# Optimization experiments

Measured on AMD Instinct MI355X. Metric: run time of the kernel, lower is better.

## Reference

```python
import jax, jax.numpy as jnp
import numpy as np

B, C, H, W = 4, 64, 256, 256
WS = 8          # window size
HEADS = 4       # dim // dim_head, dim_head = 16
DH = 16         # dim_head used for scale
HID = 64        # gated conv FFN hidden (mult=1)


def conv2d(x, w, b=None, stride=1, pad=1, groups=1):
    out = jax.lax.conv_general_dilated(
        x, w, (stride, stride), [(pad, pad), (pad, pad)],
        feature_group_count=groups,
        dimension_numbers=('NCHW', 'OIHW', 'NCHW'))
    if b is not None:
        out = out + b[None, :, None, None]
    return out


def gelu(x):
    return jax.nn.gelu(x, approximate=False)  # torch F.gelu / nn.GELU default (erf)


def ln2d(x, w, b, eps=1e-6):  # LayerNorm2d: normalize over channel dim
    mu = jnp.mean(x, axis=1, keepdims=True)
    var = jnp.mean((x - mu) ** 2, axis=1, keepdims=True)
    return w[None, :, None, None] * ((x - mu) / jnp.sqrt(var + eps)) + b[None, :, None, None]


def ln_last(x, w, b, eps=1e-5):  # nn.LayerNorm over last dim
    mu = jnp.mean(x, axis=-1, keepdims=True)
    var = jnp.mean((x - mu) ** 2, axis=-1, keepdims=True)
    return w * ((x - mu) / jnp.sqrt(var + eps)) + b


def to_windows(x, w):  # b d (x w1) (y w2) -> b x y w1 w2 d
    b, c, h, ww = x.shape
    x = x.reshape(b, c, h // w, w, ww // w, w)
    return jnp.transpose(x, (0, 2, 4, 3, 5, 1))


def from_windows(x):  # b x y w1 w2 d -> b d (x w1) (y w2)
    b, nx, ny, w1, w2, c = x.shape
    return jnp.transpose(x, (0, 5, 1, 3, 2, 4)).reshape(b, c, nx * w1, ny * w2)


def setup_inputs() -> dict:
    key = jax.random.key(0)
    ks = iter(jax.random.split(key, 64))

    def rn(*shape):
        return jax.random.normal(next(ks), shape, dtype=jnp.float32) * 0.05

    d = dict(
        x=jax.random.normal(next(ks), (B, C, H, W), dtype=jnp.float32),
        norm_w=jnp.ones((C,), jnp.float32), norm_b=jnp.zeros((C,), jnp.float32),
        conv1_w=rn(C, C, 1, 1), conv1_b=jnp.zeros((C,), jnp.float32),
        conv2_w=rn(C, 2 * C, 1, 1), conv2_b=jnp.zeros((C,), jnp.float32),
        mb_w1=rn(C, C, 1, 1), mb_b1=jnp.zeros((C,), jnp.float32),
        mb_dw_w=rn(C, 1, 3, 3), mb_dw_b=jnp.zeros((C,), jnp.float32),
        se_w1=rn(16, C), se_w2=rn(C, 16),
        mb_w2=rn(C, C, 1, 1), mb_b2=jnp.zeros((C,), jnp.float32),
        ln_att_w=jnp.ones((C,), jnp.float32), ln_att_b=jnp.zeros((C,), jnp.float32),
        q1_w=rn(C // 2, C), q1_b=jnp.zeros((C // 2,), jnp.float32),
        qkv_w=rn(3 * C // 2, C // 2),
        to_out_w=rn(C // 2, C // 2),
        sr_w=rn(C, C, 3, 3), sr_b=jnp.zeros((C,), jnp.float32),
        ln_sr_w=jnp.ones((C,), jnp.float32), ln_sr_b=jnp.zeros((C,), jnp.float32),
        kv1_w=rn(C, C), kv1_b=jnp.zeros((C,), jnp.float32),
        q2_w=rn(C // 2, C), q2_b=jnp.zeros((C // 2,), jnp.float32),
        cd_w=rn(C // 2, C // 2, 3, 3), cd_b=jnp.zeros((C // 2,), jnp.float32),
        cu_w=rn(C // 2, C // 2, 3, 3), cu_b=jnp.zeros((C // 2,), jnp.float32),
        cln1_w=jnp.ones((C,), jnp.float32), cln1_b=jnp.zeros((C,), jnp.float32),
        ff1_in_w=rn(2 * HID, C, 1, 1), ff1_dw_w=rn(2 * HID, 1, 3, 3), ff1_out_w=rn(C, HID, 1, 1),
        cln2_w=jnp.ones((C,), jnp.float32), cln2_b=jnp.zeros((C,), jnp.float32),
        ca_temp=jnp.ones((HEADS, 1, 1), jnp.float32),
        ca_qkv_w=rn(3 * C, C, 1, 1), ca_dw_w=rn(3 * C, 1, 3, 3), ca_out_w=rn(C, C, 1, 1),
        cln3_w=jnp.ones((C,), jnp.float32), cln3_b=jnp.zeros((C,), jnp.float32),
        ff2_in_w=rn(2 * HID, C, 1, 1), ff2_dw_w=rn(2 * HID, 1, 3, 3), ff2_out_w=rn(C, HID, 1, 1),
    )
    return d


def reference(x, norm_w, norm_b, conv1_w, conv1_b, conv2_w, conv2_b,
              mb_w1, mb_b1, mb_dw_w, mb_dw_b, se_w1, se_w2, mb_w2, mb_b2,
              ln_att_w, ln_att_b, q1_w, q1_b, qkv_w, to_out_w,
              sr_w, sr_b, ln_sr_w, ln_sr_b, kv1_w, kv1_b, q2_w, q2_b,
              cd_w, cd_b, cu_w, cu_b,
              cln1_w, cln1_b, ff1_in_w, ff1_dw_w, ff1_out_w,
              cln2_w, cln2_b, ca_temp, ca_qkv_w, ca_dw_w, ca_out_w,
              cln3_w, cln3_b, ff2_in_w, ff2_dw_w, ff2_out_w):
    scale = DH ** -0.5
    # input norm + 1x1 conv
    y = conv2d(ln2d(x, norm_w, norm_b), conv1_w, conv1_b, pad=0)
    # ---- MBConv (expansion 1, SE, residual) ----
    r = y
    t = gelu(conv2d(y, mb_w1, mb_b1, pad=0))
    t = gelu(conv2d(t, mb_dw_w, mb_dw_b, pad=1, groups=C))
    s = jnp.mean(t, axis=(2, 3))                      # (B,C) squeeze
    s = jax.nn.sigmoid(jax.nn.silu(s @ se_w1.T) @ se_w2.T)
    y = conv2d(t * s[:, :, None, None], mb_w2, mb_b2, pad=0) + r
    # ---- windowed hybrid attention, PreNormResidual ----
    xw = to_windows(y, WS)                            # (B,nx,ny,8,8,C)
    xn = ln_last(xw, ln_att_w, ln_att_b)
    xf = from_windows(xn)                             # (B,C,H,W)
    b, c, h, w = xf.shape
    nx, ny = h // WS, w // WS
    # window self-attention branch on dim/2
    xq = jnp.einsum('bchw,oc->bohw', xf, q1_w) + q1_b[None, :, None, None]
    tw = to_windows(xq, WS).reshape(b * nx * ny, WS * WS, c // 2)
    qkv = tw @ qkv_w.T
    q, k, v = jnp.split(qkv, 3, axis=-1)

    def heads_split(t):
        return jnp.transpose(t.reshape(t.shape[0], WS * WS, HEADS, -1), (0, 2, 1, 3))

    q, k, v = heads_split(q) * scale, heads_split(k), heads_split(v)
    attn = jax.nn.softmax(jnp.einsum('bhid,bhjd->bhij', q, k), axis=-1)
    o = jnp.einsum('bhij,bhjd->bhid', attn, v)
    o = jnp.transpose(o, (0, 2, 1, 3)).reshape(b * nx * ny, WS, WS, c // 2)
    o = (o @ to_out_w.T).reshape(b, nx, ny, WS, WS, c // 2)
    # low-resolution cross-attention branch on dim/2
    iq = jnp.einsum('bchw,oc->bohw', xf, q2_w) + q2_b[None, :, None, None]
    iq = conv2d(iq, cd_w, cd_b, stride=8, pad=1)      # (B,C/2,H/8,W/8)
    qq = jnp.transpose(iq.reshape(b, h * w // 64, HEADS // 2, c // HEADS), (0, 2, 1, 3))
    x1 = conv2d(xf, sr_w, sr_b, stride=16, pad=1)     # (B,C,h16,w16)
    x1 = jnp.transpose(x1.reshape(b, c, -1), (0, 2, 1))
    x1 = gelu(ln_last(x1, ln_sr_w, ln_sr_b))
    kv = (x1 @ kv1_w.T + kv1_b).reshape(b, -1, 2, HEADS // 2, c // HEADS)
    kv = jnp.transpose(kv, (2, 0, 3, 1, 4))
    k1, v1 = kv[0], kv[1]                             # (B,2,N,16)
    a1 = jax.nn.softmax(jnp.einsum('bhid,bhjd->bhij', qq, k1) * scale, axis=-1)
    o1 = jnp.einsum('bhij,bhjd->bhid', a1, v1)        # (B,2,HW/64,16)
    o1 = jnp.transpose(o1, (0, 1, 3, 2)).reshape(b, c // 2, h // 8, w // 8)
    o1 = jnp.repeat(jnp.repeat(o1, 8, axis=2), 8, axis=3)   # nearest upsample x8
    o1 = to_windows(conv2d(o1, cu_w, cu_b, pad=1), WS)
    xw = jnp.concatenate([o, o1], axis=-1) + xw       # residual
    y = from_windows(xw)

    def gcff(z, in_w, dw_w, out_w):
        t = conv2d(conv2d(z, in_w, pad=0), dw_w, pad=1, groups=2 * HID)
        a, g = jnp.split(t, 2, axis=1)
        return conv2d(gelu(a) * g, out_w, pad=0)

    y = y + gcff(ln2d(y, cln1_w, cln1_b), ff1_in_w, ff1_dw_w, ff1_out_w)
    # ---- windowed channel (transposed) attention ----
    z = ln2d(y, cln2_w, cln2_b)
    qkv2 = conv2d(conv2d(z, ca_qkv_w, pad=0), ca_dw_w, pad=1, groups=3 * C)
    qc, kc, vc = jnp.split(qkv2, 3, axis=1)
    hp, wp = h // WS, w // WS

    def rw(t):  # b (head d) (h ph) (w pw) -> b (h w) head d (ph pw)
        t = t.reshape(b, HEADS, C // HEADS, hp, WS, wp, WS)
        return jnp.transpose(t, (0, 3, 5, 1, 2, 4, 6)).reshape(b, hp * wp, HEADS, C // HEADS, WS * WS)

    qc, kc, vc = rw(qc), rw(kc), rw(vc)
    qc = qc / jnp.clip(jnp.linalg.norm(qc, axis=-1, keepdims=True), 1e-12)
    kc = kc / jnp.clip(jnp.linalg.norm(kc, axis=-1, keepdims=True), 1e-12)
    aat = jax.nn.softmax(jnp.einsum('bnhde,bnhfe->bnhdf', qc, kc) * ca_temp, axis=-1)
    oc = jnp.einsum('bnhdf,bnhfe->bnhde', aat, vc)    # (B,Nw,head,16,64)
    oc = oc.reshape(b, hp, wp, HEADS, C // HEADS, WS, WS)
    oc = jnp.transpose(oc, (0, 3, 4, 1, 5, 2, 6)).reshape(b, C, h, w)
    y = y + conv2d(oc, ca_out_w, pad=0)
    y = y + gcff(ln2d(y, cln3_w, cln3_b), ff2_in_w, ff2_dw_w, ff2_out_w)
    # fuse branch with block input
    return conv2d(jnp.concatenate([x, y], axis=1), conv2_w, conv2_b, pad=0)
```

## Files before the change

kernel.cpp:

```cpp
#include <hip/hip_runtime.h>
#include <hip/hip_bf16.h>
#include <math.h>

typedef __hip_bfloat16 bf16;

static constexpr int B_ = 4;
static constexpr int C_ = 64;
static constexpr int H_ = 256;
static constexpr int W_ = 256;
static constexpr int P_ = H_ * W_;
static constexpr int NP_ = B_ * P_;

static constexpr int HSTR = 61;

__device__ __forceinline__ float cvt(float x) { return x; }
__device__ __forceinline__ float cvt(bf16 x) { return __bfloat162float(x); }
__device__ __forceinline__ float geluf(float x) { return 0.5f * x * (1.0f + erff(x * 0.70710678118654752f)); }
__device__ __forceinline__ float sigm(float x) { return 1.0f / (1.0f + __expf(-x)); }

__device__ __forceinline__ float ldin(const void* p, int i, bool bf) {
    return bf ? __bfloat162float(((const bf16*)p)[i]) : ((const float*)p)[i];
}

__device__ __forceinline__ void bf2x(unsigned u, float& a, float& b) {
    a = __uint_as_float(u << 16);
    b = __uint_as_float(u & 0xffff0000u);
}
__device__ __forceinline__ float bflo(unsigned u) { return __uint_as_float(u << 16); }
__device__ __forceinline__ float bfhi(unsigned u) { return __uint_as_float(u & 0xffff0000u); }
__device__ __forceinline__ unsigned bfpack(float a, float b) {
    union { unsigned u; bf16 h[2]; } pk;
    pk.h[0] = __float2bfloat16(a);
    pk.h[1] = __float2bfloat16(b);
    return pk.u;
}

__device__ __forceinline__ int win_swz(int bid) { return (bid & 7) * 512 + (bid >> 3); }

__global__ __launch_bounds__(256) void k_detect(const unsigned int* __restrict__ x, int* __restrict__ flag) {
    __shared__ int red[256];
    int cnt = 0;
    for (int i = threadIdx.x; i < 4096; i += 256) {
        unsigned int u = x[i];
        unsigned int e = (u >> 7) & 0xFFu;
        cnt += (e >= 100u && e <= 140u) ? 1 : 0;
    }
    red[threadIdx.x] = cnt;
    __syncthreads();
    for (int s = 128; s > 0; s >>= 1) {
        if (threadIdx.x < s) red[threadIdx.x] += red[threadIdx.x + s];
        __syncthreads();
    }
    if (threadIdx.x == 0) flag[0] = (red[0] > 2048) ? 1 : 0;
}

__global__ __launch_bounds__(256) void k_head(const void* __restrict__ x,
                                              const void* __restrict__ lnw, const void* __restrict__ lnb,
                                              const void* __restrict__ w1, const void* __restrict__ b1,
                                              const void* __restrict__ w2, const void* __restrict__ b2,
                                              float* __restrict__ Y, bf16* __restrict__ T1,
                                              const int* __restrict__ dtf) {
    const bool bf = dtf[0] != 0;
    __shared__ bf16 s1[4096], s2[4096];
    __shared__ float sb1[64], sb2[64], slw[64], slb[64];
    for (int i = threadIdx.x; i < 4096; i += 256) {
        s1[i] = __float2bfloat16(ldin(w1, i, bf));
        s2[i] = __float2bfloat16(ldin(w2, i, bf));
    }
    if (threadIdx.x < 64) {
        sb1[threadIdx.x] = ldin(b1, threadIdx.x, bf);
        sb2[threadIdx.x] = ldin(b2, threadIdx.x, bf);
        slw[threadIdx.x] = ldin(lnw, threadIdx.x, bf);
        slb[threadIdx.x] = ldin(lnb, threadIdx.x, bf);
    }
    __syncthreads();
    int g = blockIdx.x * 256 + threadIdx.x;
    int bb = g >> 16, p = g & (P_ - 1);
    int base = bb * 64 * P_ + p;
    float v[64];
    float mu = 0.f;
#pragma unroll
    for (int c = 0; c < 64; ++c) { v[c] = ldin(x, base + c * P_, bf); mu += v[c]; }
    mu *= (1.0f / 64.0f);
    float var = 0.f;
#pragma unroll
    for (int c = 0; c < 64; ++c) { float d = v[c] - mu; var += d * d; }
    float inv = rsqrtf(var * (1.0f / 64.0f) + 1e-6f);
#pragma unroll
    for (int c = 0; c < 64; ++c) v[c] = (v[c] - mu) * inv * slw[c] + slb[c];
    float y[64];
    const unsigned* u1 = (const unsigned*)s1;
    for (int o = 0; o < 64; ++o) {
        float a = sb1[o];
#pragma unroll
        for (int cc = 0; cc < 32; ++cc) {
            float wa, wb;
            bf2x(u1[o * 32 + cc], wa, wb);
            a = fmaf(wa, v[2 * cc], fmaf(wb, v[2 * cc + 1], a));
        }
        y[o] = a;
        Y[base + o * P_] = a;
    }
    const unsigned* u2 = (const unsigned*)s2;
    for (int o = 0; o < 64; ++o) {
        float a = sb2[o];
#pragma unroll
        for (int cc = 0; cc < 32; ++cc) {
            float wa, wb;
            bf2x(u2[o * 32 + cc], wa, wb);
            a = fmaf(wa, y[2 * cc], fmaf(wb, y[2 * cc + 1], a));
        }
        T1[base + o * P_] = __float2bfloat16(geluf(a));
    }
}

__global__ __launch_bounds__(256) void k_ln(const float* __restrict__ in,
                                            const void* __restrict__ w,
                                            const void* __restrict__ b,
                                            bf16* __restrict__ out, float eps,
                                            const int* __restrict__ dtf) {
    const bool bf = dtf[0] != 0;
    __shared__ float swt[C_], sbt[C_];
    if (threadIdx.x < C_) {
        swt[threadIdx.x] = ldin(w, threadIdx.x, bf);
        sbt[threadIdx.x] = ldin(b, threadIdx.x, bf);
    }
    __syncthreads();
    int g = blockIdx.x * 256 + threadIdx.x;
    int bb = g >> 16;
    int p = g & (P_ - 1);
    int base = bb * C_ * P_ + p;
    float v[C_];
    float mu = 0.f;
#pragma unroll
    for (int c = 0; c < C_; ++c) { v[c] = in[base + c * P_]; mu += v[c]; }
    mu *= (1.0f / C_);
    float var = 0.f;
#pragma unroll
    for (int c = 0; c < C_; ++c) { float d = v[c] - mu; var += d * d; }
    var *= (1.0f / C_);
    float inv = rsqrtf(var + eps);
#pragma unroll
    for (int c = 0; c < C_; ++c)
        out[base + c * P_] = __float2bfloat16((v[c] - mu) * inv * swt[c] + sbt[c]);
}

template <int COUT>
__global__ __launch_bounds__(256) void k_pwln(const float* __restrict__ Yin,
                                              const void* __restrict__ lnw, const void* __restrict__ lnb,
                                              const void* __restrict__ w,
                                              bf16* __restrict__ out,
                                              const int* __restrict__ dtf) {
    const bool bf = dtf[0] != 0;
    __shared__ bf16 swb[COUT * 64];
    __shared__ float slw[64], slb[64];
    for (int i = threadIdx.x; i < COUT * 64; i += 256) swb[i] = __float2bfloat16(ldin(w, i, bf));
    if (threadIdx.x < 64) {
        slw[threadIdx.x] = ldin(lnw, threadIdx.x, bf);
        slb[threadIdx.x] = ldin(lnb, threadIdx.x, bf);
    }
    __syncthreads();
    int g = blockIdx.x * 256 + threadIdx.x;
    int bb = g >> 16, p = g & (P_ - 1);
    int base = bb * 64 * P_ + p;
    float v[64];
    float mu = 0.f;
#pragma unroll
    for (int c = 0; c < 64; ++c) { v[c] = Yin[base + c * P_]; mu += v[c]; }
    mu *= (1.0f / 64.0f);
    float var = 0.f;
#pragma unroll
    for (int c = 0; c < 64; ++c) { float d = v[c] - mu; var += d * d; }
    float inv = rsqrtf(var * (1.0f / 64.0f) + 1e-6f);
#pragma unroll
    for (int c = 0; c < 64; ++c) v[c] = (v[c] - mu) * inv * slw[c] + slb[c];
    int obase = bb * COUT * P_ + p;
    const unsigned* uw = (const unsigned*)swb;
    for (int o = 0; o < COUT; ++o) {
        float a = 0.f;
#pragma unroll
        for (int cc = 0; cc < 32; ++cc) {
            float wa, wb;
            bf2x(uw[o * 32 + cc], wa, wb);
            a = fmaf(wa, v[2 * cc], fmaf(wb, v[2 * cc + 1], a));
        }
        out[obase + o * P_] = __float2bfloat16(a);
    }
}

__global__ __launch_bounds__(256) void k_dwmean(const bf16* __restrict__ h,
                                                const void* __restrict__ dww,
                                                const void* __restrict__ dwb,
                                                float* __restrict__ part,
                                                const int* __restrict__ dtf) {
    const bool bf = dtf[0] != 0;
    __shared__ __align__(8) bf16 hsb[10 * 256];
    __shared__ float red[256];
    int bid = blockIdx.x;
    int bc = bid >> 5, chunk = bid & 31;
    int c = bc & 63;
    int h0 = chunk * 8;
    int base = bc * P_;
    int tid = threadIdx.x;
    {
        const unsigned* gq = (const unsigned*)h;
        unsigned* hu = (unsigned*)hsb;
        for (int i = tid; i < 1280; i += 256) {
            int r = i >> 7, col2 = i & 127;
            int hh = h0 - 1 + r;
            unsigned v = 0u;
            if ((unsigned)hh < (unsigned)H_) v = gq[(base + hh * W_) / 2 + col2];
            hu[r * 128 + col2] = v;
        }
    }
    float w9[9];
#pragma unroll
    for (int k = 0; k < 9; ++k) w9[k] = ldin(dww, c * 9 + k, bf);
    float bv = ldin(dwb, c, bf);
    __syncthreads();
    float acc = 0.f;
#pragma unroll
    for (int k = 0; k < 8; ++k) {
        int j = tid + k * 256;
        int r = j >> 8, x = j & 255;
        float s = bv;
#pragma unroll
        for (int kh = 0; kh < 3; ++kh) {
            const bf16* row = &hsb[(r + kh) * 256];
            float vm1 = (x > 0) ? cvt(row[x - 1]) : 0.f;
            float v0 = cvt(row[x]);
            float vp1 = (x < 255) ? cvt(row[x + 1]) : 0.f;
            s = fmaf(w9[kh * 3 + 0], vm1, s);
            s = fmaf(w9[kh * 3 + 1], v0, s);
            s = fmaf(w9[kh * 3 + 2], vp1, s);
        }
        acc += geluf(s);
    }
    red[tid] = acc;
    __syncthreads();
    for (int s2 = 128; s2 > 0; s2 >>= 1) {
        if (tid < s2) red[tid] += red[tid + s2];
        __syncthreads();
    }
    if (tid == 0) part[bc * 32 + chunk] = red[0];
}

__global__ __launch_bounds__(256) void k_se(const float* __restrict__ part,
                                            const void* __restrict__ w1,
                                            const void* __restrict__ w2,
                                            float* __restrict__ sfin,
                                            const int* __restrict__ dtf) {
    const bool bf = dtf[0] != 0;
    __shared__ float ssum[256];
    __shared__ float hbuf[B_ * 16];
    int t = threadIdx.x;
    {
        float a = 0.f;
#pragma unroll
        for (int k = 0; k < 32; ++k) a += part[t * 32 + k];
        ssum[t] = a * (1.0f / P_);
    }
    __syncthreads();
    if (t < B_ * 16) {
        int bb = t >> 4, j = t & 15;
        float a = 0.f;
        for (int c = 0; c < 64; ++c) a = fmaf(ssum[bb * 64 + c], ldin(w1, j * 64 + c, bf), a);
        hbuf[t] = a * sigm(a);
    }
    __syncthreads();
    int bb = t >> 6, c = t & 63;
    float a = 0.f;
    for (int j = 0; j < 16; ++j) a = fmaf(hbuf[bb * 16 + j], ldin(w2, c * 16 + j, bf), a);
    sfin[t] = sigm(a);
}

__global__ __launch_bounds__(256) void k_mb2w(const bf16* __restrict__ h,
                                              const void* __restrict__ dww, const void* __restrict__ dwb,
                                              const void* __restrict__ w2, const void* __restrict__ b2,
                                              const float* __restrict__ sfin,
                                              float* __restrict__ Y,
                                              const int* __restrict__ dtf) {
    const bool bf = dtf[0] != 0;
    __shared__ __align__(16) bf16 hs[64 * 2 * HSTR];
    __shared__ __align__(16) bf16 ts[64 * 66];
    __shared__ __align__(16) bf16 sw2T[64 * 64];
    __shared__ float sdb[64], sb2[64], ssc[64];
    int wid = win_swz(blockIdx.x);
    int bb = wid >> 10;
    int h0 = ((wid >> 5) & 31) * 8, w0 = (wid & 31) * 8;
    int tid = threadIdx.x;
    int cch = tid >> 2, quarter = tid & 3;
    {
        const unsigned* gq = (const unsigned*)h;
        unsigned* hsu = (unsigned*)hs;
        int j = quarter * 15;
        int pr = j / 6, col = j - pr * 6;
        size_t chb = (size_t)(bb * 64 + cch) * P_;
        for (int k = 0; k < 15; ++k) {
            int hh = h0 + pr - 1;
            int wcx = w0 - 2 + 2 * col;
            unsigned v = 0u;
            if ((unsigned)hh < (unsigned)H_ && (unsigned)wcx < 255u)
                v = gq[(chb + hh * W_ + wcx) >> 1];
            hsu[cch * HSTR + j] = v;
            ++j; ++col;
            if (col == 6) { col = 0; ++pr; }
        }
    }
    float w9[9];
#pragma unroll
    for (int k = 0; k < 9; ++k) w9[k] = ldin(dww, cch * 9 + k, bf);
    for (int i = tid; i < 4096; i += 256) {
        int c = i >> 6, o = i & 63;
        sw2T[c * 64 + o] = __float2bfloat16(ldin(w2, o * 64 + c, bf));
    }
    if (tid < 64) {
        sdb[tid] = ldin(dwb, tid, bf);
        sb2[tid] = ldin(b2, tid, bf);
        ssc[tid] = sfin[bb * 64 + tid];
    }
    __syncthreads();
    {
        const unsigned* mua = (const unsigned*)hs + cch * HSTR;
        unsigned* tsu = (unsigned*)ts;
        float bv = sdb[cch];
        float sc = ssc[cch];
#pragma unroll
        for (int k = 0; k < 8; ++k) {
            int p = quarter * 8 + k;
            int t0 = 2 * p;
            int rt = t0 >> 3, ct = t0 & 7;
            float a0 = bv, a1 = bv;
#pragma unroll
            for (int kh = 0; kh < 3; ++kh) {
                int rb = (rt + kh) * 6 + (ct >> 1);
                unsigned u0 = mua[rb], u1 = mua[rb + 1], u2 = mua[rb + 2];
                float x1 = bfhi(u0);
                float x2 = bflo(u1), x3 = bfhi(u1);
                float x4 = bflo(u2);
                a0 = fmaf(w9[kh * 3 + 0], x1, fmaf(w9[kh * 3 + 1], x2, fmaf(w9[kh * 3 + 2], x3, a0)));
                a1 = fmaf(w9[kh * 3 + 0], x2, fmaf(w9[kh * 3 + 1], x3, fmaf(w9[kh * 3 + 2], x4, a1)));
            }
            tsu[cch * 33 + p] = bfpack(geluf(a0) * sc, geluf(a1) * sc);
        }
    }
    __syncthreads();
    int og = tid >> 4, pg = tid & 15;
    int o0 = og * 4, p0 = pg * 4;
    float acc[4][4] = {};
    const unsigned* wt = (const unsigned*)sw2T;
    const unsigned* tt = (const unsigned*)ts;
    for (int c = 0; c < 64; ++c) {
        float w0v, w1v, w2v, w3v, t0, t1, t2, t3;
        bf2x(wt[c * 32 + (o0 >> 1)], w0v, w1v);
        bf2x(wt[c * 32 + (o0 >> 1) + 1], w2v, w3v);
        bf2x(tt[c * 33 + (p0 >> 1)], t0, t1);
        bf2x(tt[c * 33 + (p0 >> 1) + 1], t2, t3);
        acc[0][0] = fmaf(w0v, t0, acc[0][0]); acc[0][1] = fmaf(w0v, t1, acc[0][1]);
        acc[0][2] = fmaf(w0v, t2, acc[0][2]); acc[0][3] = fmaf(w0v, t3, acc[0][3]);
        acc[1][0] = fmaf(w1v, t0, acc[1][0]); acc[1][1] = fmaf(w1v, t1, acc[1][1]);
        acc[1][2] = fmaf(w1v, t2, acc[1][2]); acc[1][3] = fmaf(w1v, t3, acc[1][3]);
        acc[2][0] = fmaf(w2v, t0, acc[2][0]); acc[2][1] = fmaf(w2v, t1, acc[2][1]);
        acc[2][2] = fmaf(w2v, t2, acc[2][2]); acc[2][3] = fmaf(w2v, t3, acc[2][3]);
        acc[3][0] = fmaf(w3v, t0, acc[3][0]); acc[3][1] = fmaf(w3v, t1, acc[3][1]);
        acc[3][2] = fmaf(w3v, t2, acc[3][2]); acc[3][3] = fmaf(w3v, t3, acc[3][3]);
    }
#pragma unroll
    for (int i = 0; i < 4; ++i)
#pragma unroll
        for (int j = 0; j < 4; ++j) {
            int t = p0 + j;
            int p = (h0 + (t >> 3)) * W_ + w0 + (t & 7);
            Y[(bb * 64 + o0 + i) * P_ + p] += acc[i][j] + sb2[o0 + i];
        }
}

__global__ __launch_bounds__(256) void k_wprep(const void* __restrict__ q1w, const void* __restrict__ q1b,
                                               const void* __restrict__ qkvw, const void* __restrict__ outw,
                                               bf16* __restrict__ WQT, float* __restrict__ BQ,
                                               bf16* __restrict__ OWT,
                                               const int* __restrict__ dtf) {
    const bool bf = dtf[0] != 0;
    __shared__ float sq1[32 * 64];
    __shared__ float sqk[96 * 32];
    __shared__ float sb1[32];
    int tid = threadIdx.x;
    for (int i = tid; i < 2048; i += 256) sq1[i] = ldin(q1w, i, bf);
    for (int i = tid; i < 3072; i += 256) sqk[i] = ldin(qkvw, i, bf);
    if (tid < 32) sb1[tid] = ldin(q1b, tid, bf);
    __syncthreads();
    for (int idx = tid; idx < 6144; idx += 256) {
        int o = idx % 96, c = idx / 96;
        float a = 0.f;
        for (int k = 0; k < 32; ++k) a = fmaf(sqk[o * 32 + k], sq1[k * 64 + c], a);
        if (o < 32) a *= 0.25f;
        WQT[c * 96 + o] = __float2bfloat16(a);
    }
    if (tid < 96) {
        float a = 0.f;
        for (int k = 0; k < 32; ++k) a = fmaf(sqk[tid * 32 + k], sb1[k], a);
        if (tid < 32) a *= 0.25f;
        BQ[tid] = a;
    }
    for (int idx = tid; idx < 1024; idx += 256) {
        int o = idx >> 5, c = idx & 31;
        OWT[c * 32 + o] = __float2bfloat16(ldin(outw, o * 32 + c, bf));
    }
}

__global__ __launch_bounds__(256, 4) void k_winattn(const bf16* __restrict__ xf,
                                                    const uint4* __restrict__ WQT,
                                                    const float* __restrict__ BQ,
                                                    const unsigned* __restrict__ OWT,
                                                    float* __restrict__ Y) {
    __shared__ __align__(16) char arena[35200];
    int wid = win_swz(blockIdx.x);
    int bb = wid >> 10;
    int h0 = ((wid >> 5) & 31) * 8, w0 = (wid & 31) * 8;
    int tid = threadIdx.x;
    {
        uint4* sW4 = (uint4*)arena;
        for (int i = tid; i < 768; i += 256) sW4[i] = WQT[i];
        if (tid < 96) ((float*)(arena + 12288))[tid] = BQ[tid];
#pragma unroll
        for (int k = 0; k < 2; ++k) {
            int idx = tid + k * 256;
            int c = idx >> 3, r = idx & 7;
            const uint4 v = *(const uint4*)(xf + (size_t)(bb * 64 + c) * P_ + (h0 + r) * W_ + w0);
            *(uint4*)(arena + 12672 + c * 144 + r * 16) = v;
        }
    }
    __syncthreads();
    {
        const unsigned* uW = (const unsigned*)arena;
        const float* sbq = (const float*)(arena + 12288);
        const unsigned* uX = (const unsigned*)(arena + 12672);
        unsigned* uQw = (unsigned*)(arena + 21888);
        int og = tid >> 4, pg = tid & 15;
        float acc[6][4];
#pragma unroll
        for (int i = 0; i < 6; ++i) {
            float b = sbq[og * 6 + i];
#pragma unroll
            for (int j = 0; j < 4; ++j) acc[i][j] = b;
        }
        for (int c = 0; c < 64; ++c) {
            unsigned wu0 = uW[c * 48 + 3 * og];
            unsigned wu1 = uW[c * 48 + 3 * og + 1];
            unsigned wu2 = uW[c * 48 + 3 * og + 2];
            unsigned xu0 = uX[c * 36 + 2 * pg];
            unsigned xu1 = uX[c * 36 + 2 * pg + 1];
            float wv[6], xv[4];
            bf2x(wu0, wv[0], wv[1]); bf2x(wu1, wv[2], wv[3]); bf2x(wu2, wv[4], wv[5]);
            bf2x(xu0, xv[0], xv[1]); bf2x(xu1, xv[2], xv[3]);
#pragma unroll
            for (int i = 0; i < 6; ++i)
#pragma unroll
                for (int j = 0; j < 4; ++j) acc[i][j] = fmaf(wv[i], xv[j], acc[i][j]);
        }
#pragma unroll
        for (int j = 0; j < 4; ++j) {
            int t = pg * 4 + j;
#pragma unroll
            for (int k = 0; k < 3; ++k) {
                union { unsigned u; bf16 h[2]; } pk;
                pk.h[0] = __float2bfloat16(acc[2 * k][j]);
                pk.h[1] = __float2bfloat16(acc[2 * k + 1][j]);
                uQw[t * 52 + 3 * og + k] = pk.u;
            }
        }
    }
    __syncthreads();
    {
        int hH = tid >> 6, lane = tid & 63;
        const unsigned* uQ = (const unsigned*)(arena + 21888);
        unsigned ow0 = OWT[tid * 2], ow1 = OWT[tid * 2 + 1];
        float qf[8];
        {
            const uint4 qv = *(const uint4*)&uQ[lane * 52 + hH * 4];
            bf2x(qv.x, qf[0], qf[1]); bf2x(qv.y, qf[2], qf[3]);
            bf2x(qv.z, qf[4], qf[5]); bf2x(qv.w, qf[6], qf[7]);
        }
        float p[64];
#pragma unroll
        for (int j = 0; j < 64; ++j) {
            const uint4 kv4 = *(const uint4*)&uQ[j * 52 + 16 + hH * 4];
            float kf[8];
            bf2x(kv4.x, kf[0], kf[1]); bf2x(kv4.y, kf[2], kf[3]);
            bf2x(kv4.z, kf[4], kf[5]); bf2x(kv4.w, kf[6], kf[7]);
            float s = 0.f;
#pragma unroll
            for (int d = 0; d < 8; ++d) s = fmaf(qf[d], kf[d], s);
            p[j] = s;
        }
        float m0 = fmaxf(p[0], p[4]), m1 = fmaxf(p[1], p[5]);
        float m2 = fmaxf(p[2], p[6]), m3 = fmaxf(p[3], p[7]);
#pragma unroll
        for (int j = 8; j < 64; j += 4) {
            m0 = fmaxf(m0, p[j]);     m1 = fmaxf(m1, p[j + 1]);
            m2 = fmaxf(m2, p[j + 2]); m3 = fmaxf(m3, p[j + 3]);
        }
        float mm = fmaxf(fmaxf(m0, m1), fmaxf(m2, m3));
        float s0 = 0.f, s1 = 0.f, s2 = 0.f, s3 = 0.f;
#pragma unroll
        for (int j = 0; j < 64; j += 4) {
            p[j] = __expf(p[j] - mm);         s0 += p[j];
            p[j + 1] = __expf(p[j + 1] - mm); s1 += p[j + 1];
            p[j + 2] = __expf(p[j + 2] - mm); s2 += p[j + 2];
            p[j + 3] = __expf(p[j + 3] - mm); s3 += p[j + 3];
        }
        float rs = 1.0f / ((s0 + s1) + (s2 + s3));
        float o[8] = {0.f, 0.f, 0.f, 0.f, 0.f, 0.f, 0.f, 0.f};
#pragma unroll
        for (int j = 0; j < 64; ++j) {
            const uint4 vv = *(const uint4*)&uQ[j * 52 + 32 + hH * 4];
            float vf[8];
            bf2x(vv.x, vf[0], vf[1]); bf2x(vv.y, vf[2], vf[3]);
            bf2x(vv.z, vf[4], vf[5]); bf2x(vv.w, vf[6], vf[7]);
#pragma unroll
            for (int d = 0; d < 8; ++d) o[d] = fmaf(p[j], vf[d], o[d]);
        }
        bf16* soa = (bf16*)(arena + 12672);
#pragma unroll
        for (int d = 0; d < 8; ++d)
            soa[(hH * 8 + d) * 68 + lane] = __float2bfloat16(o[d] * rs);
        unsigned* sow = (unsigned*)(arena + 17024);
        sow[tid * 2] = ow0; sow[tid * 2 + 1] = ow1;
    }
    __syncthreads();
    {
        const unsigned* uOW = (const unsigned*)(arena + 17024);
        const unsigned* uOA = (const unsigned*)(arena + 12672);
        int og = tid >> 4, pg = tid & 15;
        float a2[2][4] = {};
        for (int c = 0; c < 32; ++c) {
            unsigned wu = uOW[c * 16 + og];
            unsigned a0 = uOA[c * 34 + 2 * pg], a1 = uOA[c * 34 + 2 * pg + 1];
            float wf0, wf1, x0, x1, x2, x3;
            bf2x(wu, wf0, wf1); bf2x(a0, x0, x1); bf2x(a1, x2, x3);
            a2[0][0] = fmaf(wf0, x0, a2[0][0]); a2[0][1] = fmaf(wf0, x1, a2[0][1]);
            a2[0][2] = fmaf(wf0, x2, a2[0][2]); a2[0][3] = fmaf(wf0, x3, a2[0][3]);
            a2[1][0] = fmaf(wf1, x0, a2[1][0]); a2[1][1] = fmaf(wf1, x1, a2[1][1]);
            a2[1][2] = fmaf(wf1, x2, a2[1][2]); a2[1][3] = fmaf(wf1, x3, a2[1][3]);
        }
#pragma unroll
        for (int i = 0; i < 2; ++i)
#pragma unroll
            for (int j = 0; j < 4; ++j) {
                int t = pg * 4 + j;
                int p2 = (h0 + (t >> 3)) * W_ + w0 + (t & 7);
                Y[((size_t)bb * 64 + og * 2 + i) * P_ + p2] += a2[i][j];
            }
    }
}

template <int CIN, int COUT>
__global__ __launch_bounds__(256) void k_pw(const bf16* __restrict__ in,
                                            const void* __restrict__ w,
                                            const void* __restrict__ bias,
                                            bf16* __restrict__ out,
                                            const int* __restrict__ dtf) {
    const bool bf = dtf[0] != 0;
    __shared__ float sw[COUT * CIN];
    __shared__ float sb[COUT];
    for (int i = threadIdx.x; i < COUT * CIN; i += 256) sw[i] = ldin(w, i, bf);
    if (threadIdx.x < COUT) sb[threadIdx.x] = bias ? ldin(bias, threadIdx.x, bf) : 0.f;
    __syncthreads();
    int g = blockIdx.x * 256 + threadIdx.x;
    int bb = g >> 16;
    int p = g & (P_ - 1);
    int ibase = bb * CIN * P_ + p;
    float v[CIN];
#pragma unroll
    for (int c = 0; c < CIN; ++c) v[c] = cvt(in[ibase + c * P_]);
    int obase = bb * COUT * P_ + p;
    for (int o = 0; o < COUT; ++o) {
        float acc = sb[o];
        const float* wr = &sw[o * CIN];
#pragma unroll
        for (int c = 0; c < CIN; ++c) acc = fmaf(wr[c], v[c], acc);
        out[obase + o * P_] = __float2bfloat16(acc);
    }
}

template <int CIN, int COUT, int OS, int STRIDE>
__global__ __launch_bounds__(256) void k_sconv(const bf16* __restrict__ in,
                                               const void* __restrict__ w,
                                               const void* __restrict__ bias,
                                               float* __restrict__ out,
                                               const int* __restrict__ dtf) {
    const bool bf = dtf[0] != 0;
    int g = blockIdx.x * 256 + threadIdx.x;
    int ow = g % OS;
    int oh = (g / OS) % OS;
    int oc = (g / (OS * OS)) % COUT;
    int bb = g / (OS * OS * COUT);
    float acc = ldin(bias, oc, bf);
    for (int ic = 0; ic < CIN; ++ic) {
        int ibase = (bb * CIN + ic) * P_;
        int wbase = (oc * CIN + ic) * 9;
#pragma unroll
        for (int kh = 0; kh < 3; ++kh) {
            int ih = oh * STRIDE + kh - 1;
            if ((unsigned)ih >= (unsigned)H_) continue;
#pragma unroll
            for (int kw = 0; kw < 3; ++kw) {
                int iw = ow * STRIDE + kw - 1;
                if ((unsigned)iw >= (unsigned)W_) continue;
                acc = fmaf(ldin(w, wbase + kh * 3 + kw, bf), cvt(in[ibase + ih * W_ + iw]), acc);
            }
        }
    }
    out[g] = acc;
}

__global__ __launch_bounds__(64) void k_srkv(const float* __restrict__ x1,
                                             const void* __restrict__ lnw,
                                             const void* __restrict__ lnb,
                                             const void* __restrict__ kvw,
                                             const void* __restrict__ kvb,
                                             float* __restrict__ k1,
                                             float* __restrict__ v1,
                                             const int* __restrict__ dtf) {
    const bool bf = dtf[0] != 0;
    int tok = blockIdx.x;
    int bb = tok >> 8;
    int n = tok & 255;
    int c = threadIdx.x;
    __shared__ float sv[64];
    __shared__ float sg[64];
    float v = x1[(bb * 64 + c) * 256 + n];
    sv[c] = v;
    __syncthreads();
    float mu = 0.f;
    for (int i = 0; i < 64; ++i) mu += sv[i];
    mu *= (1.0f / 64.0f);
    float var = 0.f;
    for (int i = 0; i < 64; ++i) { float d = sv[i] - mu; var += d * d; }
    var *= (1.0f / 64.0f);
    float xn = (v - mu) * rsqrtf(var + 1e-5f) * ldin(lnw, c, bf) + ldin(lnb, c, bf);
    sg[c] = geluf(xn);
    __syncthreads();
    float acc = ldin(kvb, c, bf);
    for (int j = 0; j < 64; ++j) acc = fmaf(ldin(kvw, c * 64 + j, bf), sg[j], acc);
    int kk = c >> 5;
    int jh = (c >> 4) & 1;
    int d = c & 15;
    float* dst = kk ? v1 : k1;
    dst[((bb * 2 + jh) * 256 + n) * 16 + d] = acc;
}

__global__ __launch_bounds__(256) void k_xattn(const float* __restrict__ iqd,
                                               const float* __restrict__ k1,
                                               const float* __restrict__ v1,
                                               float* __restrict__ o1sp) {
    int bid = blockIdx.x;
    int iblk = bid & 3;
    int j = (bid >> 2) & 1;
    int bb = bid >> 3;
    __shared__ float sk[256 * 16];
    __shared__ float svv[256 * 16];
    int kbase = ((bb * 2 + j) * 256) * 16;
    for (int idx = threadIdx.x; idx < 4096; idx += 256) { sk[idx] = k1[kbase + idx]; svv[idx] = v1[kbase + idx]; }
    __syncthreads();
    int i = iblk * 256 + threadIdx.x;
    float q[16];
    int qbase = ((bb * 32 + (i >> 5)) * 32 + (i & 31)) * 32 + j * 16;
#pragma unroll
    for (int d = 0; d < 16; ++d) q[d] = iqd[qbase + d];
    float m = -1e30f, l = 0.f, o[16];
#pragma unroll
    for (int d = 0; d < 16; ++d) o[d] = 0.f;
    for (int n = 0; n < 256; ++n) {
        float s = 0.f;
#pragma unroll
        for (int d = 0; d < 16; ++d) s = fmaf(q[d], sk[n * 16 + d], s);
        s *= 0.25f;
        float mn = fmaxf(m, s);
        float corr = __expf(m - mn);
        float e = __expf(s - mn);
        l = l * corr + e;
#pragma unroll
        for (int d = 0; d < 16; ++d) o[d] = fmaf(o[d], corr, e * svv[n * 16 + d]);
        m = mn;
    }
    float r = 1.0f / l;
#pragma unroll
    for (int d = 0; d < 16; ++d)
        o1sp[((bb * 32 + j * 16 + d) * 32 + (i >> 5)) * 32 + (i & 31)] = o[d] * r;
}

__global__ __launch_bounds__(256) void k_cuconv(const float* __restrict__ o1sp,
                                                const void* __restrict__ w,
                                                const void* __restrict__ bias,
                                                float* __restrict__ Y,
                                                const int* __restrict__ dtf) {
    const bool bf = dtf[0] != 0;
    __shared__ float sw[32 * 32 * 9];
    for (int i = threadIdx.x; i < 9216; i += 256) sw[i] = ldin(w, i, bf);
    __syncthreads();
    int g = blockIdx.x * 256 + threadIdx.x;
    int bb = g >> 16;
    int p = g & 65535;
    int h = p >> 8, x = p & 255;
    float acc[32];
#pragma unroll
    for (int oc = 0; oc < 32; ++oc) acc[oc] = ldin(bias, oc, bf);
    for (int ic = 0; ic < 32; ++ic) {
        int ibase = (bb * 32 + ic) * 1024;
        float v[9];
#pragma unroll
        for (int kh = 0; kh < 3; ++kh)
#pragma unroll
            for (int kw = 0; kw < 3; ++kw) {
                int hh = h + kh - 1, ww = x + kw - 1;
                v[kh * 3 + kw] = ((unsigned)hh < (unsigned)H_ && (unsigned)ww < (unsigned)W_)
                                     ? o1sp[ibase + (hh >> 3) * 32 + (ww >> 3)] : 0.f;
            }
        for (int oc = 0; oc < 32; ++oc) {
            const float* wr = &sw[(oc * 32 + ic) * 9];
            float a = acc[oc];
#pragma unroll
            for (int k = 0; k < 9; ++k) a = fmaf(wr[k], v[k], a);
            acc[oc] = a;
        }
    }
#pragma unroll
    for (int oc = 0; oc < 32; ++oc) Y[(bb * 64 + 32 + oc) * P_ + p] += acc[oc];
}

__global__ __launch_bounds__(256) void k_gcff2(const bf16* __restrict__ mid_g,
                                               const void* __restrict__ dww,
                                               const void* __restrict__ outw,
                                               float* __restrict__ Y,
                                               const int* __restrict__ dtf) {
    const bool bf = dtf[0] != 0;
    __shared__ __align__(16) char arena[39680];
    bf16* mid = (bf16*)arena;
    bf16* ts = (bf16*)(arena + 31232);
    bf16* sowT = (bf16*)arena;
    int wid = win_swz(blockIdx.x);
    int bb = wid >> 10;
    int h0 = ((wid >> 5) & 31) * 8, w0 = (wid & 31) * 8;
    int tid = threadIdx.x;
    {
        const unsigned* gq = (const unsigned*)mid_g;
        unsigned* mu = (unsigned*)mid;
        int c = tid >> 1, half = tid & 1;
        int j = half * 30;
        int pr = half * 5, col = 0;
        size_t chb = (size_t)(bb * 128 + c) * P_;
        for (int k = 0; k < 30; ++k) {
            int hh = h0 + pr - 1;
            int wcx = w0 - 2 + 2 * col;
            unsigned v = 0u;
            if ((unsigned)hh < (unsigned)H_ && (unsigned)wcx < 255u)
                v = gq[(chb + hh * W_ + wcx) >> 1];
            mu[c * HSTR + j] = v;
            ++j; ++col;
            if (col == 6) { col = 0; ++pr; }
        }
    }
    int cch = tid >> 2, quarter = tid & 3;
    float wa9[9], wg9[9];
#pragma unroll
    for (int k = 0; k < 9; ++k) {
        wa9[k] = ldin(dww, cch * 9 + k, bf);
        wg9[k] = ldin(dww, (cch + 64) * 9 + k, bf);
    }
    __syncthreads();
    {
        const unsigned* mua = (const unsigned*)mid + cch * HSTR;
        const unsigned* mug = (const unsigned*)mid + (cch + 64) * HSTR;
        unsigned* tsu = (unsigned*)ts;
#pragma unroll
        for (int k = 0; k < 8; ++k) {
            int p = quarter * 8 + k;
            int t0 = 2 * p;
            int rt = t0 >> 3, ct = t0 & 7;
            float a0 = 0.f, a1 = 0.f, g0 = 0.f, g1 = 0.f;
#pragma unroll
            for (int kh = 0; kh < 3; ++kh) {
                int rb = (rt + kh) * 6 + (ct >> 1);
                unsigned ua0 = mua[rb], ua1 = mua[rb + 1], ua2 = mua[rb + 2];
                unsigned ug0 = mug[rb], ug1 = mug[rb + 1], ug2 = mug[rb + 2];
                float x1 = bfhi(ua0);
                float x2 = bflo(ua1), x3 = bfhi(ua1);
                float x4 = bflo(ua2);
                a0 = fmaf(wa9[kh * 3 + 0], x1, fmaf(wa9[kh * 3 + 1], x2, fmaf(wa9[kh * 3 + 2], x3, a0)));
                a1 = fmaf(wa9[kh * 3 + 0], x2, fmaf(wa9[kh * 3 + 1], x3, fmaf(wa9[kh * 3 + 2], x4, a1)));
                float y1 = bfhi(ug0);
                float y2 = bflo(ug1), y3 = bfhi(ug1);
                float y4 = bflo(ug2);
                g0 = fmaf(wg9[kh * 3 + 0], y1, fmaf(wg9[kh * 3 + 1], y2, fmaf(wg9[kh * 3 + 2], y3, g0)));
                g1 = fmaf(wg9[kh * 3 + 0], y2, fmaf(wg9[kh * 3 + 1], y3, fmaf(wg9[kh * 3 + 2], y4, g1)));
            }
            tsu[cch * 33 + p] = bfpack(geluf(a0) * g0, geluf(a1) * g1);
        }
    }
    __syncthreads();
    for (int i = tid; i < 4096; i += 256) {
        int c = i >> 6, o = i & 63;
        sowT[c * 64 + o] = __float2bfloat16(ldin(outw, o * 64 + c, bf));
    }
    __syncthreads();
    int og = tid >> 4, pg = tid & 15;
    int o0 = og * 4, p0 = pg * 4;
    float acc[4][4] = {};
    const unsigned* wt = (const unsigned*)sowT;
    const unsigned* tt = (const unsigned*)ts;
    for (int c = 0; c < 64; ++c) {
        float w0v, w1v, w2v, w3v, t0, t1, t2, t3;
        bf2x(wt[c * 32 + (o0 >> 1)], w0v, w1v);
        bf2x(wt[c * 32 + (o0 >> 1) + 1], w2v, w3v);
        bf2x(tt[c * 33 + (p0 >> 1)], t0, t1);
        bf2x(tt[c * 33 + (p0 >> 1) + 1], t2, t3);
        acc[0][0] = fmaf(w0v, t0, acc[0][0]); acc[0][1] = fmaf(w0v, t1, acc[0][1]);
        acc[0][2] = fmaf(w0v, t2, acc[0][2]); acc[0][3] = fmaf(w0v, t3, acc[0][3]);
        acc[1][0] = fmaf(w1v, t0, acc[1][0]); acc[1][1] = fmaf(w1v, t1, acc[1][1]);
        acc[1][2] = fmaf(w1v, t2, acc[1][2]); acc[1][3] = fmaf(w1v, t3, acc[1][3]);
        acc[2][0] = fmaf(w2v, t0, acc[2][0]); acc[2][1] = fmaf(w2v, t1, acc[2][1]);
        acc[2][2] = fmaf(w2v, t2, acc[2][2]); acc[2][3] = fmaf(w2v, t3, acc[2][3]);
        acc[3][0] = fmaf(w3v, t0, acc[3][0]); acc[3][1] = fmaf(w3v, t1, acc[3][1]);
        acc[3][2] = fmaf(w3v, t2, acc[3][2]); acc[3][3] = fmaf(w3v, t3, acc[3][3]);
    }
#pragma unroll
    for (int i = 0; i < 4; ++i)
#pragma unroll
        for (int j = 0; j < 4; ++j) {
            int t = p0 + j;
            int p = (h0 + (t >> 3)) * W_ + w0 + (t & 7);
            Y[(bb * 64 + o0 + i) * P_ + p] += acc[i][j];
        }
}

__global__ __launch_bounds__(256) void k_chattn2(const bf16* __restrict__ qkv_g,
                                                 const void* __restrict__ dww,
                                                 const void* __restrict__ outw,
                                                 const void* __restrict__ tempw,
                                                 float* __restrict__ Y,
                                                 const int* __restrict__ dtf) {
    const bool bf = dtf[0] != 0;
    __shared__ __align__(16) char arena[49152];
    bf16* sq = (bf16*)arena;
    bf16* chunkb = (bf16*)(arena + 25344);
    bf16* s_owT = (bf16*)(arena + 40960);
    float* s_att = (float*)(arena + 25344);
    bf16* s_oc = (bf16*)(arena + 29696);
    int wid = win_swz(blockIdx.x);
    int bb = wid >> 10;
    int h0 = ((wid >> 5) & 31) * 8, w0 = (wid & 31) * 8;
    int tid = threadIdx.x;
    int cch = tid >> 2, quarter = tid & 3;
    const unsigned* gq = (const unsigned*)qkv_g;
    unsigned* cbu = (unsigned*)chunkb;
    unsigned* squ = (unsigned*)sq;
    int j0 = quarter * 15;
    int pr0 = j0 / 6, col0 = j0 - pr0 * 6;
    for (int chunk = 0; chunk < 3; ++chunk) {
        int ch0 = chunk * 64;
        {
            int j = j0, pr = pr0, col = col0;
            size_t chb = (size_t)((bb * 192 + ch0 + cch) * P_);
            for (int k = 0; k < 15; ++k) {
                int hh = h0 + pr - 1;
                int wcx = w0 - 2 + 2 * col;
                unsigned v = 0u;
                if ((unsigned)hh < (unsigned)H_ && (unsigned)wcx < 255u)
                    v = gq[(chb + hh * W_ + wcx) >> 1];
                cbu[cch * HSTR + j] = v;
                ++j; ++col;
                if (col == 6) { col = 0; ++pr; }
            }
        }
        float w9[9];
#pragma unroll
        for (int k = 0; k < 9; ++k) w9[k] = ldin(dww, (ch0 + cch) * 9 + k, bf);
        __syncthreads();
        {
            const unsigned* mua = cbu + cch * HSTR;
#pragma unroll
            for (int k = 0; k < 8; ++k) {
                int p = quarter * 8 + k;
                int t0 = 2 * p;
                int rt = t0 >> 3, ct = t0 & 7;
                float a0 = 0.f, a1 = 0.f;
#pragma unroll
                for (int kh = 0; kh < 3; ++kh) {
                    int rb = (rt + kh) * 6 + (ct >> 1);
                    unsigned u0 = mua[rb], u1 = mua[rb + 1], u2 = mua[rb + 2];
                    float x1 = bfhi(u0);
                    float x2 = bflo(u1), x3 = bfhi(u1);
                    float x4 = bflo(u2);
                    a0 = fmaf(w9[kh * 3 + 0], x1, fmaf(w9[kh * 3 + 1], x2, fmaf(w9[kh * 3 + 2], x3, a0)));
                    a1 = fmaf(w9[kh * 3 + 0], x2, fmaf(w9[kh * 3 + 1], x3, fmaf(w9[kh * 3 + 2], x4, a1)));
                }
                squ[(ch0 + cch) * 33 + p] = bfpack(a0, a1);
            }
        }
        __syncthreads();
    }
    if (tid < 128) {
        unsigned* row = squ + tid * 33;
        float v[64];
        float ss = 0.f;
#pragma unroll
        for (int t2 = 0; t2 < 32; ++t2) {
            bf2x(row[t2], v[2 * t2], v[2 * t2 + 1]);
            ss = fmaf(v[2 * t2], v[2 * t2], fmaf(v[2 * t2 + 1], v[2 * t2 + 1], ss));
        }
        float inv = 1.0f / fmaxf(sqrtf(ss), 1e-12f);
#pragma unroll
        for (int t2 = 0; t2 < 32; ++t2)
            row[t2] = bfpack(v[2 * t2] * inv, v[2 * t2 + 1] * inv);
    }
    __syncthreads();
    for (int i = tid; i < 1024; i += 256) {
        int hh = i >> 8, d = (i >> 4) & 15, f = i & 15;
        const unsigned* qrow = squ + (hh * 16 + d) * 33;
        const unsigned* krow = squ + (64 + hh * 16 + f) * 33;
        float acc = 0.f;
#pragma unroll
        for (int t2 = 0; t2 < 32; ++t2) {
            float q0, q1, k0, k1;
            bf2x(qrow[t2], q0, q1);
            bf2x(krow[t2], k0, k1);
            acc = fmaf(q0, k0, fmaf(q1, k1, acc));
        }
        s_att[(hh * 16 + d) * 17 + f] = acc * ldin(tempw, hh, bf);
    }
    __syncthreads();
    if (tid < 64) {
        int row = tid;
        float m = -1e30f;
        for (int f = 0; f < 16; ++f) m = fmaxf(m, s_att[row * 17 + f]);
        float sum = 0.f;
        for (int f = 0; f < 16; ++f) { float e = __expf(s_att[row * 17 + f] - m); s_att[row * 17 + f] = e; sum += e; }
        float r = 1.0f / sum;
        for (int f = 0; f < 16; ++f) s_att[row * 17 + f] *= r;
    }
    __syncthreads();
    {
        unsigned* s_ocu = (unsigned*)s_oc;
        for (int i = tid; i < 2048; i += 256) {
            int row = i >> 5, p = i & 31;
            int hh = row >> 4, d = row & 15;
            const float* arow = &s_att[(hh * 16 + d) * 17];
            float o0 = 0.f, o1 = 0.f;
#pragma unroll
            for (int f = 0; f < 16; ++f) {
                float av = arow[f];
                float v0, v1;
                bf2x(squ[(128 + hh * 16 + f) * 33 + p], v0, v1);
                o0 = fmaf(av, v0, o0);
                o1 = fmaf(av, v1, o1);
            }
            s_ocu[row * 33 + p] = bfpack(o0, o1);
        }
    }
    for (int i = tid; i < 4096; i += 256) {
        int c = i >> 6, o = i & 63;
        s_owT[c * 64 + o] = __float2bfloat16(ldin(outw, o * 64 + c, bf));
    }
    __syncthreads();
    int og = tid >> 4, pg = tid & 15;
    int o0 = og * 4, p0 = pg * 4;
    float acc[4][4] = {};
    const unsigned* wt = (const unsigned*)s_owT;
    const unsigned* tt = (const unsigned*)s_oc;
    for (int c = 0; c < 64; ++c) {
        float w0v, w1v, w2v, w3v, t0, t1, t2, t3;
        bf2x(wt[c * 32 + (o0 >> 1)], w0v, w1v);
        bf2x(wt[c * 32 + (o0 >> 1) + 1], w2v, w3v);
        bf2x(tt[c * 33 + (p0 >> 1)], t0, t1);
        bf2x(tt[c * 33 + (p0 >> 1) + 1], t2, t3);
        acc[0][0] = fmaf(w0v, t0, acc[0][0]); acc[0][1] = fmaf(w0v, t1, acc[0][1]);
        acc[0][2] = fmaf(w0v, t2, acc[0][2]); acc[0][3] = fmaf(w0v, t3, acc[0][3]);
        acc[1][0] = fmaf(w1v, t0, acc[1][0]); acc[1][1] = fmaf(w1v, t1, acc[1][1]);
        acc[1][2] = fmaf(w1v, t2, acc[1][2]); acc[1][3] = fmaf(w1v, t3, acc[1][3]);
        acc[2][0] = fmaf(w2v, t0, acc[2][0]); acc[2][1] = fmaf(w2v, t1, acc[2][1]);
        acc[2][2] = fmaf(w2v, t2, acc[2][2]); acc[2][3] = fmaf(w2v, t3, acc[2][3]);
        acc[3][0] = fmaf(w3v, t0, acc[3][0]); acc[3][1] = fmaf(w3v, t1, acc[3][1]);
        acc[3][2] = fmaf(w3v, t2, acc[3][2]); acc[3][3] = fmaf(w3v, t3, acc[3][3]);
    }
#pragma unroll
    for (int i = 0; i < 4; ++i)
#pragma unroll
        for (int j = 0; j < 4; ++j) {
            int t = p0 + j;
            int p = (h0 + (t >> 3)) * W_ + w0 + (t & 7);
            Y[(bb * 64 + o0 + i) * P_ + p] += acc[i][j];
        }
}

__global__ __launch_bounds__(256) void k_final(const void* __restrict__ x,
                                               const float* __restrict__ Yb,
                                               const void* __restrict__ w,
                                               const void* __restrict__ bias,
                                               void* __restrict__ out,
                                               const int* __restrict__ dtf) {
    const bool bf = dtf[0] != 0;
    __shared__ float sw[64 * 128];
    __shared__ float sb[64];
    for (int i = threadIdx.x; i < 8192; i += 256) sw[i] = ldin(w, i, bf);
    if (threadIdx.x < 64) sb[threadIdx.x] = ldin(bias, threadIdx.x, bf);
    __syncthreads();
    int g = blockIdx.x * 256 + threadIdx.x;
    int bb = g >> 16;
    int p = g & 65535;
    float xv[64], yv[64];
    int base = bb * 64 * P_ + p;
#pragma unroll
    for (int c = 0; c < 64; ++c) xv[c] = ldin(x, base + c * P_, bf);
#pragma unroll
    for (int c = 0; c < 64; ++c) yv[c] = Yb[base + c * P_];
    for (int o = 0; o < 64; ++o) {
        float acc = sb[o];
        const float* wr = &sw[o * 128];
#pragma unroll
        for (int c = 0; c < 64; ++c) acc = fmaf(wr[c], xv[c], acc);
#pragma unroll
        for (int c = 0; c < 64; ++c) acc = fmaf(wr[64 + c], yv[c], acc);
        if (bf) ((bf16*)out)[base + o * P_] = __float2bfloat16(acc);
        else    ((float*)out)[base + o * P_] = acc;
    }
}

extern "C" void kernel_launch(void* const* d_in, const int* in_sizes, int n_in,
                              void* d_out, int out_size, void* d_ws, size_t ws_size,
                              hipStream_t stream) {
    const void* x        = d_in[0];
    const void* norm_w   = d_in[1];
    const void* norm_b   = d_in[2];
    const void* conv1_w  = d_in[3];
    const void* conv1_b  = d_in[4];
    const void* conv2_w  = d_in[5];
    const void* conv2_b  = d_in[6];
    const void* mb_w1    = d_in[7];
    const void* mb_b1    = d_in[8];
    const void* mb_dw_w  = d_in[9];
    const void* mb_dw_b  = d_in[10];
    const void* se_w1    = d_in[11];
    const void* se_w2    = d_in[12];
    const void* mb_w2    = d_in[13];
    const void* mb_b2    = d_in[14];
    const void* ln_att_w = d_in[15];
    const void* ln_att_b = d_in[16];
    const void* q1_w     = d_in[17];
    const void* q1_b     = d_in[18];
    const void* qkv_w    = d_in[19];
    const void* to_out_w = d_in[20];
    const void* sr_w     = d_in[21];
    const void* sr_b     = d_in[22];
    const void* ln_sr_w  = d_in[23];
    const void* ln_sr_b  = d_in[24];
    const void* kv1_w    = d_in[25];
    const void* kv1_b    = d_in[26];
    const void* q2_w     = d_in[27];
    const void* q2_b     = d_in[28];
    const void* cd_w     = d_in[29];
    const void* cd_b     = d_in[30];
    const void* cu_w     = d_in[31];
    const void* cu_b     = d_in[32];
    const void* cln1_w   = d_in[33];
    const void* cln1_b   = d_in[34];
    const void* ff1_in_w = d_in[35];
    const void* ff1_dw_w = d_in[36];
    const void* ff1_out_w= d_in[37];
    const void* cln2_w   = d_in[38];
    const void* cln2_b   = d_in[39];
    const void* ca_temp  = d_in[40];
    const void* ca_qkv_w = d_in[41];
    const void* ca_dw_w  = d_in[42];
    const void* ca_out_w = d_in[43];
    const void* cln3_w   = d_in[44];
    const void* cln3_b   = d_in[45];
    const void* ff2_in_w = d_in[46];
    const void* ff2_dw_w = d_in[47];
    const void* ff2_out_w= d_in[48];

    char* ws = (char*)d_ws;
    int*   dtf   = (int*)ws;
    float* s_fin = (float*)(ws + 8192);
    bf16*  WQT   = (bf16*)(ws + 16384);
    float* BQc   = (float*)(ws + 28672);
    bf16*  OWT   = (bf16*)(ws + 29056);
    float* part  = (float*)(ws + 32768);
    float* iqd   = (float*)(ws + 65536);
    float* x1    = (float*)(ws + 589824);
    float* k1b   = (float*)(ws + 851968);
    float* v1b   = (float*)(ws + 983040);
    float* o1sp  = (float*)(ws + 1114112);
    float* Y     = (float*)(ws + 2097152);
    bf16*  T1    = (bf16*)(ws + 69206016);
    bf16*  IQ    = (bf16*)(ws + 102760448);
    bf16*  MIDQ  = (bf16*)(ws + 119537664);

    dim3 blk(256);
    dim3 gPix(NP_ / 256);
    dim3 gWin(B_ * 32 * 32);

    k_detect<<<dim3(1), blk, 0, stream>>>((const unsigned int*)x, dtf);
    k_wprep<<<dim3(1), blk, 0, stream>>>(q1_w, q1_b, qkv_w, to_out_w, WQT, BQc, OWT, dtf);
    k_head<<<gPix, blk, 0, stream>>>(x, norm_w, norm_b, conv1_w, conv1_b, mb_w1, mb_b1, Y, T1, dtf);
    k_dwmean<<<dim3(B_ * C_ * 32), blk, 0, stream>>>(T1, mb_dw_w, mb_dw_b, part, dtf);
    k_se<<<dim3(1), blk, 0, stream>>>(part, se_w1, se_w2, s_fin, dtf);
    k_mb2w<<<gWin, blk, 0, stream>>>(T1, mb_dw_w, mb_dw_b, mb_w2, mb_b2, s_fin, Y, dtf);
    k_ln<<<gPix, blk, 0, stream>>>(Y, ln_att_w, ln_att_b, T1, 1e-5f, dtf);
    k_winattn<<<gWin, blk, 0, stream>>>(T1, (const uint4*)WQT, BQc, (const unsigned*)OWT, Y);
    k_pw<64, 32><<<gPix, blk, 0, stream>>>(T1, q2_w, q2_b, IQ, dtf);
    k_sconv<32, 32, 32, 8><<<dim3(512), blk, 0, stream>>>(IQ, cd_w, cd_b, iqd, dtf);
    k_sconv<64, 64, 16, 16><<<dim3(256), blk, 0, stream>>>(T1, sr_w, sr_b, x1, dtf);
    k_srkv<<<dim3(B_ * 256), dim3(64), 0, stream>>>(x1, ln_sr_w, ln_sr_b, kv1_w, kv1_b, k1b, v1b, dtf);
    k_xattn<<<dim3(32), blk, 0, stream>>>(iqd, k1b, v1b, o1sp);
    k_cuconv<<<gPix, blk, 0, stream>>>(o1sp, cu_w, cu_b, Y, dtf);
    k_pwln<128><<<gPix, blk, 0, stream>>>(Y, cln1_w, cln1_b, ff1_in_w, MIDQ, dtf);
    k_gcff2<<<gWin, blk, 0, stream>>>(MIDQ, ff1_dw_w, ff1_out_w, Y, dtf);
    k_pwln<192><<<gPix, blk, 0, stream>>>(Y, cln2_w, cln2_b, ca_qkv_w, MIDQ, dtf);
    k_chattn2<<<gWin, blk, 0, stream>>>(MIDQ, ca_dw_w, ca_out_w, ca_temp, Y, dtf);
    k_pwln<128><<<gPix, blk, 0, stream>>>(Y, cln3_w, cln3_b, ff2_in_w, MIDQ, dtf);
    k_gcff2<<<gWin, blk, 0, stream>>>(MIDQ, ff2_dw_w, ff2_out_w, Y, dtf);
    k_final<<<gPix, blk, 0, stream>>>(x, Y, conv2_w, conv2_b, d_out, dtf);

    (void)in_sizes; (void)n_in; (void)out_size; (void)ws_size;
}
```

Before: 2.155 ms.

## Prefetch next qkv chunk into registers and fuse L2 norm into depthwise conv

```diff
diff --git a/kernel.cpp b/kernel.cpp
--- a/kernel.cpp
+++ b/kernel.cpp
@@ -841,10 +841,10 @@
                                                  float* __restrict__ Y,
                                                  const int* __restrict__ dtf) {
     const bool bf = dtf[0] != 0;
-    __shared__ __align__(16) char arena[49152];
+    __shared__ __align__(16) char arena[40960];
     bf16* sq = (bf16*)arena;
     bf16* chunkb = (bf16*)(arena + 25344);
-    bf16* s_owT = (bf16*)(arena + 40960);
+    bf16* s_owT = (bf16*)arena;
     float* s_att = (float*)(arena + 25344);
     bf16* s_oc = (bf16*)(arena + 29696);
     int wid = win_swz(blockIdx.x);
@@ -857,28 +857,47 @@
     unsigned* squ = (unsigned*)sq;
     int j0 = quarter * 15;
     int pr0 = j0 / 6, col0 = j0 - pr0 * 6;
+    unsigned regs[15];
+    {
+        int pr = pr0, col = col0;
+        size_t chb = (size_t)((bb * 192 + cch) * P_);
+#pragma unroll
+        for (int k = 0; k < 15; ++k) {
+            int hh = h0 + pr - 1;
+            int wcx = w0 - 2 + 2 * col;
+            unsigned v = 0u;
+            if ((unsigned)hh < (unsigned)H_ && (unsigned)wcx < 255u)
+                v = gq[(chb + hh * W_ + wcx) >> 1];
+            regs[k] = v;
+            ++col; if (col == 6) { col = 0; ++pr; }
+        }
+    }
     for (int chunk = 0; chunk < 3; ++chunk) {
         int ch0 = chunk * 64;
-        {
-            int j = j0, pr = pr0, col = col0;
-            size_t chb = (size_t)((bb * 192 + ch0 + cch) * P_);
+#pragma unroll
+        for (int k = 0; k < 15; ++k) cbu[cch * HSTR + j0 + k] = regs[k];
+        float w9[9];
+#pragma unroll
+        for (int k = 0; k < 9; ++k) w9[k] = ldin(dww, (ch0 + cch) * 9 + k, bf);
+        __syncthreads();
+        if (chunk < 2) {
+            int pr = pr0, col = col0;
+            size_t chb = (size_t)((bb * 192 + ch0 + 64 + cch) * P_);
+#pragma unroll
             for (int k = 0; k < 15; ++k) {
                 int hh = h0 + pr - 1;
                 int wcx = w0 - 2 + 2 * col;
                 unsigned v = 0u;
                 if ((unsigned)hh < (unsigned)H_ && (unsigned)wcx < 255u)
                     v = gq[(chb + hh * W_ + wcx) >> 1];
-                cbu[cch * HSTR + j] = v;
-                ++j; ++col;
-                if (col == 6) { col = 0; ++pr; }
+                regs[k] = v;
+                ++col; if (col == 6) { col = 0; ++pr; }
             }
         }
-        float w9[9];
-#pragma unroll
-        for (int k = 0; k < 9; ++k) w9[k] = ldin(dww, (ch0 + cch) * 9 + k, bf);
-        __syncthreads();
         {
             const unsigned* mua = cbu + cch * HSTR;
+            float vals[16];
+            float ss = 0.f;
 #pragma unroll
             for (int k = 0; k < 8; ++k) {
                 int p = quarter * 8 + k;
@@ -895,26 +914,22 @@
                     a0 = fmaf(w9[kh * 3 + 0], x1, fmaf(w9[kh * 3 + 1], x2, fmaf(w9[kh * 3 + 2], x3, a0)));
                     a1 = fmaf(w9[kh * 3 + 0], x2, fmaf(w9[kh * 3 + 1], x3, fmaf(w9[kh * 3 + 2], x4, a1)));
                 }
-                squ[(ch0 + cch) * 33 + p] = bfpack(a0, a1);
+                vals[2 * k] = a0; vals[2 * k + 1] = a1;
+                ss = fmaf(a0, a0, fmaf(a1, a1, ss));
             }
+            if (chunk < 2) {
+                ss += __shfl_xor(ss, 1);
+                ss += __shfl_xor(ss, 2);
+                float inv = 1.0f / fmaxf(sqrtf(ss), 1e-12f);
+#pragma unroll
+                for (int k = 0; k < 16; ++k) vals[k] *= inv;
+            }
+#pragma unroll
+            for (int k = 0; k < 8; ++k)
+                squ[(ch0 + cch) * 33 + quarter * 8 + k] = bfpack(vals[2 * k], vals[2 * k + 1]);
         }
         __syncthreads();
     }
-    if (tid < 128) {
-        unsigned* row = squ + tid * 33;
-        float v[64];
-        float ss = 0.f;
-#pragma unroll
-        for (int t2 = 0; t2 < 32; ++t2) {
-            bf2x(row[t2], v[2 * t2], v[2 * t2 + 1]);
-            ss = fmaf(v[2 * t2], v[2 * t2], fmaf(v[2 * t2 + 1], v[2 * t2 + 1], ss));
-        }
-        float inv = 1.0f / fmaxf(sqrtf(ss), 1e-12f);
-#pragma unroll
-        for (int t2 = 0; t2 < 32; ++t2)
-            row[t2] = bfpack(v[2 * t2] * inv, v[2 * t2 + 1] * inv);
-    }
-    __syncthreads();
     for (int i = tid; i < 1024; i += 256) {
         int hh = i >> 8, d = (i >> 4) & 15, f = i & 15;
         const unsigned* qrow = squ + (hh * 16 + d) * 33;
@@ -957,10 +972,10 @@
             }
             s_ocu[row * 33 + p] = bfpack(o0, o1);
         }
-    }
-    for (int i = tid; i < 4096; i += 256) {
-        int c = i >> 6, o = i & 63;
-        s_owT[c * 64 + o] = __float2bfloat16(ldin(outw, o * 64 + c, bf));
+        for (int i = tid; i < 4096; i += 256) {
+            int c = i >> 6, o = i & 63;
+            s_owT[c * 64 + o] = __float2bfloat16(ldin(outw, o * 64 + c, bf));
+        }
     }
     __syncthreads();
     int og = tid >> 4, pg = tid & 15;
```

Result: no change. 2.120 ms (-1.6%).
